# Kernel tuning notes

Hardware: AMD Instinct MI355X
Metric: run time of the kernel (lower is better)

## Reference

```python
import jax, jax.numpy as jnp
import numpy as np

B, V, C1, C2 = 4, 256, 64, 32
H0, H1, H2, OUT = 128, 128, 256, 1


def setup_inputs() -> dict:
    key = jax.random.key(0)
    ks = jax.random.split(key, 16)
    init = lambda k, shape: (jax.random.normal(k, shape, jnp.float32) * 0.05)
    return {
        "adjacency": jax.random.randint(ks[0], (B, V, V), 0, 2, jnp.int32),
        "node_features": jax.random.normal(ks[1], (B, V, C1), jnp.float32),
        "edge_attributes": jax.random.normal(ks[2], (B, V, V, C2), jnp.float32),
        # EdgeConvE #1: MLP on concat(x_i, x_j - x_i, e_ij) -> H0 -> H0
        "ec1_W1": init(ks[3], (2 * C1 + C2, H0)), "ec1_b1": jnp.zeros((H0,), jnp.float32),
        "ec1_W2": init(ks[4], (H0, H0)), "ec1_b2": jnp.zeros((H0,), jnp.float32),
        # EdgeConvE #2: input features now H0-dim -> H1 -> H0
        "ec2_W1": init(ks[5], (2 * H0 + C2, H1)), "ec2_b1": jnp.zeros((H1,), jnp.float32),
        "ec2_W2": init(ks[6], (H1, H0)), "ec2_b2": jnp.zeros((H0,), jnp.float32),
        # pair-scoring MLP: Dense(H2, relu) -> Dense(1, sigmoid)
        "h3_W": init(ks[7], (2 * H0, H2)), "h3_b": jnp.zeros((H2,), jnp.float32),
        "out_W": init(ks[8], (H2, OUT)), "out_b": jnp.zeros((OUT,), jnp.float32),
    }


def _edge_conv_e(adj, x, e, W1, b1, W2, b2):
    # EdgeConv with edge attributes: msg_ij = MLP([x_i, x_j - x_i, e_ij]),
    # masked-max aggregation over neighbors j given by adjacency.
    Bv, Vn, C = x.shape
    xi = jnp.broadcast_to(x[:, :, None, :], (Bv, Vn, Vn, C))  # center i
    xj = jnp.broadcast_to(x[:, None, :, :], (Bv, Vn, Vn, C))  # neighbor j
    h = jnp.concatenate([xi, xj - xi, e], axis=-1)            # (B,V,V,2C+Ce)
    h = jax.nn.relu(h @ W1 + b1)
    h = jax.nn.relu(h @ W2 + b2)                               # (B,V,V,H)
    h = jnp.where(adj[..., None] > 0, h, jnp.float32(-1e9))
    out = jnp.max(h, axis=2)                                   # (B,V,H)
    return jnp.where(out <= -1e9, 0.0, out)                    # isolated nodes -> 0


def _feat_concat(x):
    # flat index i*V + j holds [x_j, x_i] (matches tf.repeat axis-0 / axis-1 trick)
    Bv, Vn, C = x.shape
    src = jnp.broadcast_to(x[:, None, :, :], (Bv, Vn, Vn, C)).reshape(Bv, Vn * Vn, C)
    tgt = jnp.broadcast_to(x[:, :, None, :], (Bv, Vn, Vn, C)).reshape(Bv, Vn * Vn, C)
    return jnp.concatenate([src, tgt], axis=-1)                # (B,V*V,2C)


def reference(adjacency, node_features, edge_attributes,
              ec1_W1, ec1_b1, ec1_W2, ec1_b2,
              ec2_W1, ec2_b1, ec2_W2, ec2_b2,
              h3_W, h3_b, out_W, out_b):
    x = _edge_conv_e(adjacency, node_features, edge_attributes, ec1_W1, ec1_b1, ec1_W2, ec1_b2)
    x = _edge_conv_e(adjacency, x, edge_attributes, ec2_W1, ec2_b1, ec2_W2, ec2_b2)
    f = _feat_concat(x)                                        # (B,V*V,2H0)
    f = jax.nn.relu(f @ h3_W + h3_b)
    f = jax.nn.sigmoid(f @ out_W + out_b)                      # (B,V*V,1)
    Bv, Vn, _ = node_features.shape
    return f.reshape(Bv, Vn, Vn)
```

## Files before the change

### kernel.cpp

```cpp
#include <hip/hip_runtime.h>
#include <math.h>

#define B_  4
#define V_  256
#define C1_ 64
#define C2_ 32
#define H0_ 128
#define H2_ 256

typedef short bf16x8 __attribute__((ext_vector_type(8)));
typedef float f32x4  __attribute__((ext_vector_type(4)));

static __device__ __forceinline__ short f2bf(float f) {
    unsigned u = __float_as_uint(f);
    u += 0x7fffu + ((u >> 16) & 1u);
    return (short)(u >> 16);
}

static __device__ __forceinline__ void prep_body(
    int idx, const float* __restrict__ W1c1, const float* __restrict__ W21,
    const float* __restrict__ W1c2, const float* __restrict__ W22,
    short* __restrict__ wsW)
{
    if (idx < 4096) {
        int n = idx >> 5, k = idx & 31;
        wsW[idx] = f2bf(W1c1[k * H0_ + n]);
    } else if (idx < 20480) {
        int t = idx - 4096; int n = t >> 7, k = t & 127;
        wsW[idx] = f2bf(W21[k * H0_ + n]);
    } else if (idx < 24576) {
        int t = idx - 20480; int n = t >> 5, k = t & 31;
        wsW[idx] = f2bf(W1c2[k * H0_ + n]);
    } else if (idx < 40960) {
        int t = idx - 24576; int n = t >> 7, k = t & 127;
        wsW[idx] = f2bf(W22[k * H0_ + n]);
    }
}

template <int CIN>
static __device__ __forceinline__ void npre_body(
    int node0, const float* __restrict__ x, const float* __restrict__ W1,
    const float* __restrict__ b1, float* __restrict__ P, float* __restrict__ Q,
    float* __restrict__ sx2)
{
    const int tid  = threadIdx.x;
    const int half = tid >> 7;
    const int n    = tid & 127;
    const int bi   = node0 + half;
    float* sx = sx2 + half * CIN;
    if (n < CIN) sx[n] = x[bi * CIN + n];
    __syncthreads();
    float accP = b1[n], accQ = 0.f;
    #pragma unroll 4
    for (int k = 0; k < CIN; k += 4) {
        float4 xv = *reinterpret_cast<const float4*>(&sx[k]);
        float wa0 = W1[(k + 0) * H0_ + n], wb0 = W1[(CIN + k + 0) * H0_ + n];
        float wa1 = W1[(k + 1) * H0_ + n], wb1 = W1[(CIN + k + 1) * H0_ + n];
        float wa2 = W1[(k + 2) * H0_ + n], wb2 = W1[(CIN + k + 2) * H0_ + n];
        float wa3 = W1[(k + 3) * H0_ + n], wb3 = W1[(CIN + k + 3) * H0_ + n];
        accP = fmaf(xv.x, wa0 - wb0, accP);  accQ = fmaf(xv.x, wb0, accQ);
        accP = fmaf(xv.y, wa1 - wb1, accP);  accQ = fmaf(xv.y, wb1, accQ);
        accP = fmaf(xv.z, wa2 - wb2, accP);  accQ = fmaf(xv.z, wb2, accQ);
        accP = fmaf(xv.w, wa3 - wb3, accP);  accQ = fmaf(xv.w, wb3, accQ);
    }
    P[bi * H0_ + n] = accP;
    Q[bi * H0_ + n] = accQ;
}

__global__ __launch_bounds__(256) void pre1_fused_k(
    const float* __restrict__ W1c1, const float* __restrict__ W21,
    const float* __restrict__ W1c2, const float* __restrict__ W22,
    short* __restrict__ wsW,
    const float* __restrict__ xf, const float* __restrict__ ec1W1,
    const float* __restrict__ ec1b1, float* __restrict__ P, float* __restrict__ Q)
{
    if (blockIdx.x < 160) {
        prep_body(blockIdx.x * 256 + threadIdx.x, W1c1, W21, W1c2, W22, wsW);
    } else {
        __shared__ __align__(16) float sx2[2 * C1_];
        npre_body<C1_>((blockIdx.x - 160) * 2, xf, ec1W1, ec1b1, P, Q, sx2);
    }
}

template <int CIN>
__global__ __launch_bounds__(256) void npre2_k(
    const float* __restrict__ x, const float* __restrict__ W1,
    const float* __restrict__ b1, float* __restrict__ P, float* __restrict__ Q)
{
    __shared__ __align__(16) float sx2[2 * CIN];
    npre_body<CIN>(blockIdx.x * 2, x, W1, b1, P, Q, sx2);
}

__global__ __launch_bounds__(256, 4) void conv_mfma_k(
    const int* __restrict__ adj, const float* __restrict__ e,
    const float* __restrict__ P, const float* __restrict__ Q,
    const short* __restrict__ W1cT, const short* __restrict__ W2T,
    const float* __restrict__ b2, float* __restrict__ out)
{
    const int bi   = blockIdx.x;
    const int b    = bi >> 8;
    const int tid  = threadIdx.x;
    const int w    = tid >> 6;
    const int lane = tid & 63;
    const int l15  = lane & 15;
    const int quad = lane >> 4;

    __shared__ int s_list[V_];
    __shared__ int s_wc[4];
    __shared__ __align__(16) short s_h1[64][136];

    const int av = adj[bi * V_ + tid];
    unsigned long long bm = __ballot(av > 0);
    if (lane == 0) s_wc[w] = __popcll(bm);
    __syncthreads();
    const int cnt = s_wc[0] + s_wc[1] + s_wc[2] + s_wc[3];
    if (av > 0) {
        int base = 0;
        #pragma unroll
        for (int k = 0; k < 4; ++k) if (k < w) base += s_wc[k];
        int pos = base + __popcll(bm & ((1ull << lane) - 1ull));
        s_list[pos] = tid;
    }
    __syncthreads();
    if (cnt == 0) { if (tid < H0_) out[bi * H0_ + tid] = 0.f; return; }

    bf16x8 B2[2][4];
    float bb[2], vmax[2];
    #pragma unroll
    for (int h = 0; h < 2; ++h) {
        const int nt = w * 2 + h;
        #pragma unroll
        for (int kk = 0; kk < 4; ++kk)
            B2[h][kk] = *(const bf16x8*)(W2T + (nt * 16 + l15) * H0_ + kk * 32 + quad * 8);
        bb[h]   = b2[nt * 16 + l15];
        vmax[h] = 0.f;
    }
    float Pp[8];
    #pragma unroll
    for (int nt = 0; nt < 8; ++nt) Pp[nt] = P[bi * H0_ + nt * 16 + l15];

    const int row0 = w * 16;

    int ta0 = row0 + l15; if (ta0 >= cnt) ta0 = cnt - 1;
    const float* er0 = e + (bi * V_ + s_list[ta0]) * C2_ + quad * 8;
    float4 e0 = *(const float4*)(er0);
    float4 e1 = *(const float4*)(er0 + 4);

    for (int t0 = 0; t0 < cnt; t0 += 64) {
        const int tb = t0 + row0;

        bf16x8 A1;
        A1[0] = f2bf(e0.x); A1[1] = f2bf(e0.y); A1[2] = f2bf(e0.z); A1[3] = f2bf(e0.w);
        A1[4] = f2bf(e1.x); A1[5] = f2bf(e1.y); A1[6] = f2bf(e1.z); A1[7] = f2bf(e1.w);

        {
            int tn = t0 + 64 + row0 + l15; if (tn >= cnt) tn = cnt - 1;
            const float* ern = e + (bi * V_ + s_list[tn]) * C2_ + quad * 8;
            e0 = *(const float4*)(ern);
            e1 = *(const float4*)(ern + 4);
        }

        f32x4 acc[8];
        #pragma unroll
        for (int nt = 0; nt < 8; ++nt) {
            bf16x8 B1 = *(const bf16x8*)(W1cT + (nt * 16 + l15) * C2_ + quad * 8);
            f32x4 z = {0.f, 0.f, 0.f, 0.f};
            acc[nt] = __builtin_amdgcn_mfma_f32_16x16x32_bf16(A1, B1, z, 0, 0, 0);
        }

        if (t0 > 0) __syncthreads();

        #pragma unroll
        for (int r = 0; r < 4; ++r) {
            int t = tb + quad * 4 + r; if (t >= cnt) t = cnt - 1;
            const float* Qr = Q + (b * V_ + s_list[t]) * H0_ + l15;
            short* dst = &s_h1[row0 + quad * 4 + r][l15];
            #pragma unroll
            for (int nt = 0; nt < 8; ++nt) {
                float v = acc[nt][r] + Pp[nt] + Qr[nt * 16];
                dst[nt * 16] = f2bf(fmaxf(v, 0.f));
            }
        }

        __syncthreads();

        #pragma unroll
        for (int mt = 0; mt < 4; ++mt) {
            f32x4 a20 = {0.f,0.f,0.f,0.f}, a21 = {0.f,0.f,0.f,0.f};
            #pragma unroll
            for (int kk = 0; kk < 4; ++kk) {
                bf16x8 A2 = *(const bf16x8*)(&s_h1[mt * 16 + l15][kk * 32 + quad * 8]);
                a20 = __builtin_amdgcn_mfma_f32_16x16x32_bf16(A2, B2[0][kk], a20, 0, 0, 0);
                a21 = __builtin_amdgcn_mfma_f32_16x16x32_bf16(A2, B2[1][kk], a21, 0, 0, 0);
            }
            float m0 = fmaxf(fmaxf(a20[0], a20[1]), fmaxf(a20[2], a20[3]));
            float m1 = fmaxf(fmaxf(a21[0], a21[1]), fmaxf(a21[2], a21[3]));
            vmax[0] = fmaxf(vmax[0], fmaxf(m0 + bb[0], 0.f));
            vmax[1] = fmaxf(vmax[1], fmaxf(m1 + bb[1], 0.f));
        }
    }

    #pragma unroll
    for (int h = 0; h < 2; ++h) {
        float p = vmax[h];
        p = fmaxf(p, __shfl_xor(p, 16, 64));
        p = fmaxf(p, __shfl_xor(p, 32, 64));
        if (quad == 0) out[bi * H0_ + (w * 2 + h) * 16 + l15] = p;
    }
}

__global__ __launch_bounds__(256) void ppre2_k(
    const float* __restrict__ x2, const float* __restrict__ W3,
    const float* __restrict__ b3, float* __restrict__ Ai, float* __restrict__ Aj)
{
    const int nb = blockIdx.x;
    const int n  = threadIdx.x;
    __shared__ __align__(16) float s_x[2 * H0_];
    s_x[n] = x2[nb * 2 * H0_ + n];
    __syncthreads();
    const float bv = b3[n];
    float aI0 = bv, aJ0 = 0.f, aI1 = bv, aJ1 = 0.f;
    #pragma unroll 4
    for (int k = 0; k < H0_; k += 4) {
        float4 x0 = *reinterpret_cast<const float4*>(&s_x[k]);
        float4 x1 = *reinterpret_cast<const float4*>(&s_x[H0_ + k]);
        float wj0 = W3[(k + 0) * H2_ + n];
        float wj1 = W3[(k + 1) * H2_ + n];
        float wj2 = W3[(k + 2) * H2_ + n];
        float wj3 = W3[(k + 3) * H2_ + n];
        float wi0 = W3[(H0_ + k + 0) * H2_ + n];
        float wi1 = W3[(H0_ + k + 1) * H2_ + n];
        float wi2 = W3[(H0_ + k + 2) * H2_ + n];
        float wi3 = W3[(H0_ + k + 3) * H2_ + n];
        aJ0 = fmaf(x0.x, wj0, aJ0); aJ0 = fmaf(x0.y, wj1, aJ0);
        aJ0 = fmaf(x0.z, wj2, aJ0); aJ0 = fmaf(x0.w, wj3, aJ0);
        aI0 = fmaf(x0.x, wi0, aI0); aI0 = fmaf(x0.y, wi1, aI0);
        aI0 = fmaf(x0.z, wi2, aI0); aI0 = fmaf(x0.w, wi3, aI0);
        aJ1 = fmaf(x1.x, wj0, aJ1); aJ1 = fmaf(x1.y, wj1, aJ1);
        aJ1 = fmaf(x1.z, wj2, aJ1); aJ1 = fmaf(x1.w, wj3, aJ1);
        aI1 = fmaf(x1.x, wi0, aI1); aI1 = fmaf(x1.y, wi1, aI1);
        aI1 = fmaf(x1.z, wi2, aI1); aI1 = fmaf(x1.w, wi3, aI1);
    }
    const int r0 = nb * 2;
    Ai[r0 * H2_ + n]       = aI0;
    Aj[r0 * H2_ + n]       = aJ0;
    Ai[(r0 + 1) * H2_ + n] = aI1;
    Aj[(r0 + 1) * H2_ + n] = aJ1;
}

__global__ __launch_bounds__(256) void pair_out_k(
    const float* __restrict__ Ai, const float* __restrict__ Aj,
    const float* __restrict__ Wo, const float* __restrict__ bo,
    float* __restrict__ out)
{
    const int blk  = blockIdx.x;
    const int b    = blk >> 9;
    const int ig   = (blk >> 3) & 63;
    const int jq   = blk & 7;
    const int i    = (ig << 2) + (threadIdx.x >> 6);
    const int lane = threadIdx.x & 63;
    const int jj   = lane >> 4;
    const int c    = lane & 15;

    __shared__ __align__(16) float4 s_aj[32 * 64];

    const float4* src = (const float4*)(Aj + (b * V_ + jq * 32) * H2_);
    #pragma unroll
    for (int k = 0; k < 8; ++k) {
        int g  = threadIdx.x + k * 256;
        int jr = g >> 6, f = g & 63;
        s_aj[jr * 64 + (f ^ (jr & 7))] = src[g];
    }

    const float* ai = Ai + (b * V_ + i) * H2_ + c * 16;
    float4 a0 = *(const float4*)(ai);
    float4 a1 = *(const float4*)(ai + 4);
    float4 a2 = *(const float4*)(ai + 8);
    float4 a3 = *(const float4*)(ai + 12);
    const float* wo = Wo + c * 16;
    float4 w0 = *(const float4*)(wo);
    float4 w1 = *(const float4*)(wo + 4);
    float4 w2 = *(const float4*)(wo + 8);
    float4 w3 = *(const float4*)(wo + 12);
    const float bo0 = bo[0];

    __syncthreads();

    for (int js = 0; js < 32; js += 4) {
        const int jr = js + jj;
        const float4* arow = &s_aj[jr * 64];
        const int sw = jr & 7, f0 = c * 4;
        float4 q0 = arow[(f0 + 0) ^ sw];
        float4 q1 = arow[(f0 + 1) ^ sw];
        float4 q2 = arow[(f0 + 2) ^ sw];
        float4 q3 = arow[(f0 + 3) ^ sw];
        float p;
        p = fmaxf(a0.x + q0.x, 0.f) * w0.x;
        p = fmaf(fmaxf(a0.y + q0.y, 0.f), w0.y, p);
        p = fmaf(fmaxf(a0.z + q0.z, 0.f), w0.z, p);
        p = fmaf(fmaxf(a0.w + q0.w, 0.f), w0.w, p);
        p = fmaf(fmaxf(a1.x + q1.x, 0.f), w1.x, p);
        p = fmaf(fmaxf(a1.y + q1.y, 0.f), w1.y, p);
        p = fmaf(fmaxf(a1.z + q1.z, 0.f), w1.z, p);
        p = fmaf(fmaxf(a1.w + q1.w, 0.f), w1.w, p);
        p = fmaf(fmaxf(a2.x + q2.x, 0.f), w2.x, p);
        p = fmaf(fmaxf(a2.y + q2.y, 0.f), w2.y, p);
        p = fmaf(fmaxf(a2.z + q2.z, 0.f), w2.z, p);
        p = fmaf(fmaxf(a2.w + q2.w, 0.f), w2.w, p);
        p = fmaf(fmaxf(a3.x + q3.x, 0.f), w3.x, p);
        p = fmaf(fmaxf(a3.y + q3.y, 0.f), w3.y, p);
        p = fmaf(fmaxf(a3.z + q3.z, 0.f), w3.z, p);
        p = fmaf(fmaxf(a3.w + q3.w, 0.f), w3.w, p);
        #pragma unroll
        for (int off = 1; off < 16; off <<= 1)
            p += __shfl_xor(p, off, 64);
        if (c == 0)
            out[(b * V_ + i) * V_ + jq * 32 + jr] =
                1.f / (1.f + __builtin_expf(-(p + bo0)));
    }
}

extern "C" void kernel_launch(void* const* d_in, const int* in_sizes, int n_in,
                              void* d_out, int out_size, void* d_ws, size_t ws_size,
                              hipStream_t stream) {
    const int*   adj   = (const int*)  d_in[0];
    const float* xf    = (const float*)d_in[1];
    const float* ea    = (const float*)d_in[2];
    const float* ec1W1 = (const float*)d_in[3];
    const float* ec1b1 = (const float*)d_in[4];
    const float* ec1W2 = (const float*)d_in[5];
    const float* ec1b2 = (const float*)d_in[6];
    const float* ec2W1 = (const float*)d_in[7];
    const float* ec2b1 = (const float*)d_in[8];
    const float* ec2W2 = (const float*)d_in[9];
    const float* ec2b2 = (const float*)d_in[10];
    const float* h3W   = (const float*)d_in[11];
    const float* h3b   = (const float*)d_in[12];
    const float* oW    = (const float*)d_in[13];
    const float* ob    = (const float*)d_in[14];
    float* out = (float*)d_out;

    const int NV = B_ * V_;
    float* x1 = (float*)d_ws;
    float* x2 = x1 + NV * H0_;
    float* R  = x2 + NV * H0_;
    float* P  = R;
    float* Q  = R + NV * H0_;
    float* Ai = R;
    float* Aj = R + NV * H2_;
    short* wsW = (short*)(R + 2 * NV * H2_);
    short* W1cT1 = wsW;
    short* W2T1  = wsW + 4096;
    short* W1cT2 = wsW + 20480;
    short* W2T2  = wsW + 24576;

    pre1_fused_k<<<672, 256, 0, stream>>>(ec1W1 + 2 * C1_ * H0_, ec1W2,
                                          ec2W1 + 2 * H0_ * H0_, ec2W2, wsW,
                                          xf, ec1W1, ec1b1, P, Q);
    conv_mfma_k<<<NV, 256, 0, stream>>>(adj, ea, P, Q, W1cT1, W2T1, ec1b2, x1);
    npre2_k<H0_><<<512, 256, 0, stream>>>(x1, ec2W1, ec2b1, P, Q);
    conv_mfma_k<<<NV, 256, 0, stream>>>(adj, ea, P, Q, W1cT2, W2T2, ec2b2, x2);
    ppre2_k<<<512, 256, 0, stream>>>(x2, h3W, h3b, Ai, Aj);
    pair_out_k<<<2048, 256, 0, stream>>>(Ai, Aj, oW, ob, out);
}
```

Measured before the change: 185.6 us.

## Split each node's neighbor list across two blocks and merge partial maxes downstream

The edge-conv kernel now launches two blocks per node, and each block processes half of the node's neighbor list, writing a partial max row. The consumer kernels (npre2h_k and ppre2h_k) take the elementwise max of the two partial rows when they load their inputs. This doubles the grid to 2048 blocks and halves the serial loop length per block, aiming for better occupancy and load balance across CUs. The cost is duplicated adjacency scanning and weight loads per block, plus doubled intermediate buffers. Because outputs are clamped at zero after ReLU, an empty half contributes 0, so isolated-node semantics are preserved.

```diff
diff --git a/kernel.cpp b/kernel.cpp
--- a/kernel.cpp
+++ b/kernel.cpp
@@ -82,22 +82,44 @@
     }
 }
 
-template <int CIN>
-__global__ __launch_bounds__(256) void npre2_k(
-    const float* __restrict__ x, const float* __restrict__ W1,
+__global__ __launch_bounds__(256) void npre2h_k(
+    const float* __restrict__ xh, const float* __restrict__ W1,
     const float* __restrict__ b1, float* __restrict__ P, float* __restrict__ Q)
 {
-    __shared__ __align__(16) float sx2[2 * CIN];
-    npre_body<CIN>(blockIdx.x * 2, x, W1, b1, P, Q, sx2);
+    const int tid  = threadIdx.x;
+    const int half = tid >> 7;
+    const int n    = tid & 127;
+    const int bi   = blockIdx.x * 2 + half;
+    __shared__ __align__(16) float sx2[2 * H0_];
+    float* sx = sx2 + half * H0_;
+    sx[n] = fmaxf(xh[(bi * 2 + 0) * H0_ + n], xh[(bi * 2 + 1) * H0_ + n]);
+    __syncthreads();
+    float accP = b1[n], accQ = 0.f;
+    #pragma unroll 4
+    for (int k = 0; k < H0_; k += 4) {
+        float4 xv = *reinterpret_cast<const float4*>(&sx[k]);
+        float wa0 = W1[(k + 0) * H0_ + n], wb0 = W1[(H0_ + k + 0) * H0_ + n];
+        float wa1 = W1[(k + 1) * H0_ + n], wb1 = W1[(H0_ + k + 1) * H0_ + n];
+        float wa2 = W1[(k + 2) * H0_ + n], wb2 = W1[(H0_ + k + 2) * H0_ + n];
+        float wa3 = W1[(k + 3) * H0_ + n], wb3 = W1[(H0_ + k + 3) * H0_ + n];
+        accP = fmaf(xv.x, wa0 - wb0, accP);  accQ = fmaf(xv.x, wb0, accQ);
+        accP = fmaf(xv.y, wa1 - wb1, accP);  accQ = fmaf(xv.y, wb1, accQ);
+        accP = fmaf(xv.z, wa2 - wb2, accP);  accQ = fmaf(xv.z, wb2, accQ);
+        accP = fmaf(xv.w, wa3 - wb3, accP);  accQ = fmaf(xv.w, wb3, accQ);
+    }
+    P[bi * H0_ + n] = accP;
+    Q[bi * H0_ + n] = accQ;
 }
 
 __global__ __launch_bounds__(256, 4) void conv_mfma_k(
     const int* __restrict__ adj, const float* __restrict__ e,
     const float* __restrict__ P, const float* __restrict__ Q,
     const short* __restrict__ W1cT, const short* __restrict__ W2T,
-    const float* __restrict__ b2, float* __restrict__ out)
-{
-    const int bi   = blockIdx.x;
+    const float* __restrict__ b2, float* __restrict__ outh)
+{
+    const int blk  = blockIdx.x;
+    const int bi   = blk >> 1;
+    const int sh   = blk & 1;
     const int b    = bi >> 8;
     const int tid  = threadIdx.x;
     const int w    = tid >> 6;
@@ -122,18 +144,23 @@
         s_list[pos] = tid;
     }
     __syncthreads();
-    if (cnt == 0) { if (tid < H0_) out[bi * H0_ + tid] = 0.f; return; }
+
+    const int h  = (cnt + 1) >> 1;
+    const int lo = sh * h;
+    const int hi = min(lo + h, cnt);
+    float* orow = outh + blk * H0_;
+    if (hi <= lo) { if (tid < H0_) orow[tid] = 0.f; return; }
 
     bf16x8 B2[2][4];
     float bb[2], vmax[2];
     #pragma unroll
-    for (int h = 0; h < 2; ++h) {
-        const int nt = w * 2 + h;
+    for (int hh = 0; hh < 2; ++hh) {
+        const int nt = w * 2 + hh;
         #pragma unroll
         for (int kk = 0; kk < 4; ++kk)
-            B2[h][kk] = *(const bf16x8*)(W2T + (nt * 16 + l15) * H0_ + kk * 32 + quad * 8);
-        bb[h]   = b2[nt * 16 + l15];
-        vmax[h] = 0.f;
+            B2[hh][kk] = *(const bf16x8*)(W2T + (nt * 16 + l15) * H0_ + kk * 32 + quad * 8);
+        bb[hh]   = b2[nt * 16 + l15];
+        vmax[hh] = 0.f;
     }
     float Pp[8];
     #pragma unroll
@@ -141,12 +168,12 @@
 
     const int row0 = w * 16;
 
-    int ta0 = row0 + l15; if (ta0 >= cnt) ta0 = cnt - 1;
+    int ta0 = lo + row0 + l15; if (ta0 >= hi) ta0 = hi - 1;
     const float* er0 = e + (bi * V_ + s_list[ta0]) * C2_ + quad * 8;
     float4 e0 = *(const float4*)(er0);
     float4 e1 = *(const float4*)(er0 + 4);
 
-    for (int t0 = 0; t0 < cnt; t0 += 64) {
+    for (int t0 = lo; t0 < hi; t0 += 64) {
         const int tb = t0 + row0;
 
         bf16x8 A1;
@@ -154,7 +181,7 @@
         A1[4] = f2bf(e1.x); A1[5] = f2bf(e1.y); A1[6] = f2bf(e1.z); A1[7] = f2bf(e1.w);
 
         {
-            int tn = t0 + 64 + row0 + l15; if (tn >= cnt) tn = cnt - 1;
+            int tn = t0 + 64 + row0 + l15; if (tn >= hi) tn = hi - 1;
             const float* ern = e + (bi * V_ + s_list[tn]) * C2_ + quad * 8;
             e0 = *(const float4*)(ern);
             e1 = *(const float4*)(ern + 4);
@@ -168,11 +195,11 @@
             acc[nt] = __builtin_amdgcn_mfma_f32_16x16x32_bf16(A1, B1, z, 0, 0, 0);
         }
 
-        if (t0 > 0) __syncthreads();
+        if (t0 > lo) __syncthreads();
 
         #pragma unroll
         for (int r = 0; r < 4; ++r) {
-            int t = tb + quad * 4 + r; if (t >= cnt) t = cnt - 1;
+            int t = tb + quad * 4 + r; if (t >= hi) t = hi - 1;
             const float* Qr = Q + (b * V_ + s_list[t]) * H0_ + l15;
             short* dst = &s_h1[row0 + quad * 4 + r][l15];
             #pragma unroll
@@ -201,22 +228,27 @@
     }
 
     #pragma unroll
-    for (int h = 0; h < 2; ++h) {
-        float p = vmax[h];
+    for (int hh = 0; hh < 2; ++hh) {
+        float p = vmax[hh];
         p = fmaxf(p, __shfl_xor(p, 16, 64));
         p = fmaxf(p, __shfl_xor(p, 32, 64));
-        if (quad == 0) out[bi * H0_ + (w * 2 + h) * 16 + l15] = p;
-    }
-}
-
-__global__ __launch_bounds__(256) void ppre2_k(
-    const float* __restrict__ x2, const float* __restrict__ W3,
+        if (quad == 0) orow[(w * 2 + hh) * 16 + l15] = p;
+    }
+}
+
+__global__ __launch_bounds__(256) void ppre2h_k(
+    const float* __restrict__ x2h, const float* __restrict__ W3,
     const float* __restrict__ b3, float* __restrict__ Ai, float* __restrict__ Aj)
 {
     const int nb = blockIdx.x;
     const int n  = threadIdx.x;
     __shared__ __align__(16) float s_x[2 * H0_];
-    s_x[n] = x2[nb * 2 * H0_ + n];
+    {
+        const int node = nb * 2 + (n >> 7);
+        const int ch   = n & 127;
+        s_x[n] = fmaxf(x2h[(node * 2 + 0) * H0_ + ch],
+                       x2h[(node * 2 + 1) * H0_ + ch]);
+    }
     __syncthreads();
     const float bv = b3[n];
     float aI0 = bv, aJ0 = 0.f, aI1 = bv, aJ1 = 0.f;
@@ -341,14 +373,13 @@
     float* out = (float*)d_out;
 
     const int NV = B_ * V_;
-    float* x1 = (float*)d_ws;
-    float* x2 = x1 + NV * H0_;
-    float* R  = x2 + NV * H0_;
-    float* P  = R;
-    float* Q  = R + NV * H0_;
-    float* Ai = R;
-    float* Aj = R + NV * H2_;
-    short* wsW = (short*)(R + 2 * NV * H2_);
+    float* x1h = (float*)d_ws;
+    float* x2h = x1h + NV * 2 * H0_;
+    float* P   = x2h + NV * 2 * H0_;
+    float* Q   = P  + NV * H0_;
+    float* Ai  = Q  + NV * H0_;
+    float* Aj  = Ai + NV * H2_;
+    short* wsW = (short*)(Aj + NV * H2_);
     short* W1cT1 = wsW;
     short* W2T1  = wsW + 4096;
     short* W1cT2 = wsW + 20480;
@@ -357,9 +388,11 @@
     pre1_fused_k<<<672, 256, 0, stream>>>(ec1W1 + 2 * C1_ * H0_, ec1W2,
                                           ec2W1 + 2 * H0_ * H0_, ec2W2, wsW,
                                           xf, ec1W1, ec1b1, P, Q);
-    conv_mfma_k<<<NV, 256, 0, stream>>>(adj, ea, P, Q, W1cT1, W2T1, ec1b2, x1);
-    npre2_k<H0_><<<512, 256, 0, stream>>>(x1, ec2W1, ec2b1, P, Q);
-    conv_mfma_k<<<NV, 256, 0, stream>>>(adj, ea, P, Q, W1cT2, W2T2, ec2b2, x2);
-    ppre2_k<<<512, 256, 0, stream>>>(x2, h3W, h3b, Ai, Aj);
+    conv_mfma_k<<<2 * NV, 256, 0, stream>>>(adj, ea, P, Q, W1cT1, W2T1,
+                                            ec1b2, x1h);
+    npre2h_k<<<512, 256, 0, stream>>>(x1h, ec2W1, ec2b1, P, Q);
+    conv_mfma_k<<<2 * NV, 256, 0, stream>>>(adj, ea, P, Q, W1cT2, W2T2,
+                                            ec2b2, x2h);
+    ppre2h_k<<<512, 256, 0, stream>>>(x2h, h3W, h3b, Ai, Aj);
     pair_out_k<<<2048, 256, 0, stream>>>(Ai, Aj, oW, ob, out);
 }
```

After: 208.7 us. 1.12x slower.
